# Kernel optimization log

Hardware: AMD Instinct MI355X
Metric: run time of the kernel (lower is better)

The kernel has to match this reference:

```python
import jax, jax.numpy as jnp
import numpy as np

N_EMBD = 1024
N_HEAD = 16
B, T = 2, 2048
LN_EPS = 1e-5


def _linear_params(key, d_in, d_out):
    k1, k2 = jax.random.split(key)
    bound = 1.0 / np.sqrt(d_in)
    W = jax.random.uniform(k1, (d_in, d_out), jnp.float32, -bound, bound)
    b = jax.random.uniform(k2, (d_out,), jnp.float32, -bound, bound)
    return W, b


def setup_inputs() -> dict:
    key = jax.random.key(0)
    ks = jax.random.split(key, 8)
    x = jax.random.normal(ks[0], (B, T, N_EMBD), jnp.float32)
    Wq, bq = _linear_params(ks[1], N_EMBD, N_EMBD)
    Wk, bk = _linear_params(ks[2], N_EMBD, N_EMBD)
    Wv, bv = _linear_params(ks[3], N_EMBD, N_EMBD)
    Wo, bo = _linear_params(ks[4], N_EMBD, N_EMBD)
    W1, b1 = _linear_params(ks[5], N_EMBD, 4 * N_EMBD)
    W2, b2 = _linear_params(ks[6], 4 * N_EMBD, N_EMBD)
    ln1_g = jnp.ones((N_EMBD,), jnp.float32)
    ln1_b = jnp.zeros((N_EMBD,), jnp.float32)
    ln2_g = jnp.ones((N_EMBD,), jnp.float32)
    ln2_b = jnp.zeros((N_EMBD,), jnp.float32)
    return dict(x=x, Wq=Wq, bq=bq, Wk=Wk, bk=bk, Wv=Wv, bv=bv, Wo=Wo, bo=bo,
                W1=W1, b1=b1, W2=W2, b2=b2,
                ln1_g=ln1_g, ln1_b=ln1_b, ln2_g=ln2_g, ln2_b=ln2_b)


def _layernorm(x, g, b):
    mu = jnp.mean(x, axis=-1, keepdims=True)
    var = jnp.mean(jnp.square(x - mu), axis=-1, keepdims=True)
    return (x - mu) * jax.lax.rsqrt(var + LN_EPS) * g + b


def _attention(x, Wq, bq, Wk, bk, Wv, bv, Wo, bo):
    Bsz, Tlen, C = x.shape
    hd = C // N_HEAD
    q = (x @ Wq + bq).reshape(Bsz, Tlen, N_HEAD, hd)
    k = (x @ Wk + bk).reshape(Bsz, Tlen, N_HEAD, hd)
    v = (x @ Wv + bv).reshape(Bsz, Tlen, N_HEAD, hd)
    scale = 1.0 / np.sqrt(hd)
    # NOTE: the original module's mask buffer is all ones -> masked_fill is a
    # no-op, so attention is FULL (non-causal) despite the class name.
    att = jnp.einsum('bqhd,bkhd->bhqk', q, k) * scale
    att = jax.nn.softmax(att, axis=-1)
    y = jnp.einsum('bhqk,bkhd->bqhd', att, v).reshape(Bsz, Tlen, C)
    return y @ Wo + bo


def reference(x, Wq, bq, Wk, bk, Wv, bv, Wo, bo, W1, b1, W2, b2,
              ln1_g, ln1_b, ln2_g, ln2_b):
    x = x + _attention(_layernorm(x, ln1_g, ln1_b), Wq, bq, Wk, bk, Wv, bv, Wo, bo)
    h = _layernorm(x, ln2_g, ln2_b)
    h = jax.nn.gelu(h @ W1 + b1, approximate=False) @ W2 + b2
    return x + h
```

## Files before the change

kernel.cpp:

```cpp
#include <hip/hip_runtime.h>
#include <hip/hip_bf16.h>
#include <math.h>


typedef __bf16 bf16x8 __attribute__((ext_vector_type(8)));
typedef float f32x4 __attribute__((ext_vector_type(4)));

__device__ __forceinline__ unsigned short f2bf(float f) {
  union { float f; unsigned int u; } v; v.f = f;
  unsigned int u = v.u;
  unsigned int r = (u + 0x7fffu + ((u >> 16) & 1u)) >> 16;
  return (unsigned short)r;
}

__device__ __forceinline__ unsigned int fbits(float f) {
  union { float f; unsigned int u; } v; v.f = f;
  return v.u;
}

__device__ __forceinline__ bf16x8 ld_bf16x8(const unsigned short* p) {
  union { uint4 u; bf16x8 v; } x;
  x.u = *(const uint4*)p;
  return x.v;
}

__device__ __forceinline__ float fast_exp2(float x) {
#if __has_builtin(__builtin_amdgcn_exp2f)
  return __builtin_amdgcn_exp2f(x);
#else
  return exp2f(x);
#endif
}

__device__ __forceinline__ void async_copy16(const void* g, void* l) {
  __builtin_amdgcn_global_load_lds(
      (const __attribute__((address_space(1))) void*)g,
      (__attribute__((address_space(3))) void*)l, 16, 0, 0);
}

__global__ __launch_bounds__(256) void transpose_cast_kernel(
    const float* __restrict__ W, unsigned short* __restrict__ Wt, int N, int K) {
  __shared__ unsigned short tile[32][33];
  const int n0 = blockIdx.x * 32, k0 = blockIdx.y * 32;
  const int t = threadIdx.x;
  const int r = t >> 3, cq = (t & 7) * 4;
  float4 v = *(const float4*)&W[(size_t)(k0 + r) * N + n0 + cq];
  tile[cq + 0][r] = f2bf(v.x);
  tile[cq + 1][r] = f2bf(v.y);
  tile[cq + 2][r] = f2bf(v.z);
  tile[cq + 3][r] = f2bf(v.w);
  __syncthreads();
  ushort4 o;
  o.x = tile[r][cq + 0];
  o.y = tile[r][cq + 1];
  o.z = tile[r][cq + 2];
  o.w = tile[r][cq + 3];
  *(ushort4*)&Wt[(size_t)(n0 + r) * K + k0 + cq] = o;
}

__global__ __launch_bounds__(256) void ln_kernel(
    const float* __restrict__ x, const float* __restrict__ g,
    const float* __restrict__ b, unsigned short* __restrict__ out) {
  const int row = blockIdx.x, t = threadIdx.x;
  const float4 v = ((const float4*)(x + (size_t)row * 1024))[t];
  float s = v.x + v.y + v.z + v.w;
  float s2 = v.x * v.x + v.y * v.y + v.z * v.z + v.w * v.w;
  for (int o = 32; o > 0; o >>= 1) {
    s += __shfl_xor(s, o, 64);
    s2 += __shfl_xor(s2, o, 64);
  }
  __shared__ float red[8];
  const int w = t >> 6;
  if ((t & 63) == 0) { red[w] = s; red[4 + w] = s2; }
  __syncthreads();
  s = red[0] + red[1] + red[2] + red[3];
  s2 = red[4] + red[5] + red[6] + red[7];
  const float mu = s * (1.f / 1024.f);
  const float var = s2 * (1.f / 1024.f) - mu * mu;
  const float rs = rsqrtf(var + 1e-5f);
  const float4 gg = ((const float4*)g)[t];
  const float4 bb = ((const float4*)b)[t];
  ushort4 o4;
  o4.x = f2bf((v.x - mu) * rs * gg.x + bb.x);
  o4.y = f2bf((v.y - mu) * rs * gg.y + bb.y);
  o4.z = f2bf((v.z - mu) * rs * gg.z + bb.z);
  o4.w = f2bf((v.w - mu) * rs * gg.w + bb.w);
  ((ushort4*)(out + (size_t)row * 1024))[t] = o4;
}

enum { MODE_QKV = 0, MODE_RES = 1, MODE_GELU = 2 };

#define QSCALE 0.18033688011112043f

template <int BM, int BN, int MODE>
__global__ __launch_bounds__(256) void gemm_kernel(
    const unsigned short* __restrict__ A, const unsigned short* __restrict__ Bt,
    const float* __restrict__ bias0, const float* __restrict__ bias1,
    const float* __restrict__ bias2, const float* __restrict__ residual,
    void* __restrict__ out0, void* __restrict__ out1, void* __restrict__ out2,
    int M, int N, int K) {
  constexpr int MI = BM / 32;
  constexpr int NI = BN / 32;
  __shared__ __align__(16) unsigned short As[3][2][BM * 32];
  __shared__ __align__(16) unsigned short Bs[3][2][BN * 32];
  const int t = threadIdx.x;

  const int MT = M / BM;
  const int MTX = MT >> 3;
  const int bid = blockIdx.x;
  const int xcd = bid & 7, local = bid >> 3;
  const int mt = xcd * MTX + (local % MTX);
  const int nt_ = local / MTX;
  const int m0 = mt * BM, n0 = nt_ * BN;

  const int l = t & 63, w = t >> 6;
  const int wm = (w >> 1) * (BM / 2), wn = (w & 1) * (BN / 2);
  const int lr = l & 15, lq = l >> 4;

  f32x4 acc[MI][NI];
#pragma unroll
  for (int i = 0; i < MI; i++)
#pragma unroll
    for (int j = 0; j < NI; j++) {
      f32x4 z = {0.f, 0.f, 0.f, 0.f};
      acc[i][j] = z;
    }

  auto issue = [&](int k0, int p) {
#pragma unroll
    for (int h = 0; h < 2; h++)
#pragma unroll
      for (int s = 0; s < BM / 64; s++) {
        const int c = t + s * 256;
        const int row = c >> 2, k8 = (c & 3) * 8;
        async_copy16(&A[(size_t)(m0 + row) * K + k0 + h * 32 + k8],
                     &As[p][h][c * 8]);
      }
#pragma unroll
    for (int h = 0; h < 2; h++)
#pragma unroll
      for (int s = 0; s < BN / 64; s++) {
        const int c = t + s * 256;
        const int row = c >> 2, k8 = (c & 3) * 8;
        async_copy16(&Bt[(size_t)(n0 + row) * K + k0 + h * 32 + k8],
                     &Bs[p][h][c * 8]);
      }
  };

  issue(0, 0);
  issue(64, 1);
  int p = 0;
  for (int k0 = 0; k0 < K; k0 += 64) {
    if (k0 + 64 < K)
      asm volatile("s_waitcnt vmcnt(6)\n\ts_barrier" ::: "memory");
    else
      asm volatile("s_waitcnt vmcnt(0)\n\ts_barrier" ::: "memory");
    if (k0 + 128 < K) {
      const int pn = p >= 1 ? p - 1 : 2;
      issue(k0 + 128, pn);
    }
#pragma unroll
    for (int kk = 0; kk < 2; kk++) {
      bf16x8 af[MI], bf[NI];
#pragma unroll
      for (int mi = 0; mi < MI; mi++)
        af[mi] = ld_bf16x8(&As[p][kk][(wm + mi * 16 + lr) * 32 + lq * 8]);
#pragma unroll
      for (int ni = 0; ni < NI; ni++)
        bf[ni] = ld_bf16x8(&Bs[p][kk][(wn + ni * 16 + lr) * 32 + lq * 8]);
#pragma unroll
      for (int mi = 0; mi < MI; mi++)
#pragma unroll
        for (int ni = 0; ni < NI; ni++)
          acc[mi][ni] = __builtin_amdgcn_mfma_f32_16x16x32_bf16(
              af[mi], bf[ni], acc[mi][ni], 0, 0, 0);
    }
    p = p < 2 ? p + 1 : 0;
  }

#pragma unroll
  for (int mi = 0; mi < MI; mi++) {
#pragma unroll
    for (int ni = 0; ni < NI; ni++) {
#pragma unroll
      for (int i = 0; i < 4; i++) {
        const int gm = m0 + wm + mi * 16 + lq * 4 + i;
        const int gn = n0 + wn + ni * 16 + lr;
        const float v = acc[mi][ni][i];
        if (MODE == MODE_QKV) {
          const int sel = gn >> 10, cn = gn & 1023;
          const int hh = cn >> 6, d = cn & 63;
          const int bb2 = gm >> 11, tok = gm & 2047;
          const size_t bh = (size_t)bb2 * 16 + hh;
          float u = v + (sel == 0 ? bias0 : (sel == 1 ? bias1 : bias2))[cn];
          if (sel == 0) {
            u *= QSCALE;
            const int qt = tok >> 7, r7 = tok & 127;
            const int ww = r7 >> 5, ss = (r7 >> 4) & 1, qlr = r7 & 15;
            const int kk = d >> 5, lq2 = (d >> 3) & 3, e = d & 7;
            const size_t idx =
                (((((bh * 16 + qt) * 4 + ww) * 2 + ss) * 2 + kk) << 9) +
                (lq2 * 16 + qlr) * 8 + e;
            ((unsigned short*)out0)[idx] = f2bf(u);
          } else if (sel == 1) {
            const int ktile = tok >> 6, r6 = tok & 63;
            const int nt2 = r6 >> 4, klr = r6 & 15;
            const int kk = d >> 5, lq2 = (d >> 3) & 3, e = d & 7;
            const size_t idx =
                ((((bh * 32 + ktile) * 4 + nt2) * 2 + kk) << 9) +
                (lq2 * 16 + klr) * 8 + e;
            ((unsigned short*)out1)[idx] = f2bf(u);
          } else {
            const int ktile = tok >> 6, r6 = tok & 63;
            const int kb = r6 >> 5, lq2 = (r6 >> 3) & 3, e = r6 & 7;
            const int nt2 = d >> 4, vlr = d & 15;
            const size_t idx =
                ((((bh * 32 + ktile) * 2 + kb) * 4 + nt2) << 9) +
                (lq2 * 16 + vlr) * 8 + e;
            ((unsigned short*)out2)[idx] = f2bf(u);
          }
        } else if (MODE == MODE_RES) {
          ((float*)out0)[(size_t)gm * N + gn] =
              v + bias0[gn] + residual[(size_t)gm * N + gn];
        } else {
          const float u = v + bias0[gn];
          const float ge = 0.5f * u * (1.f + erff(u * 0.70710678118654752f));
          ((unsigned short*)out0)[(size_t)gm * N + gn] = f2bf(ge);
        }
      }
    }
  }
}

__global__ __launch_bounds__(256) void attn_kernel(
    const unsigned short* __restrict__ Qp, const unsigned short* __restrict__ Kp,
    const unsigned short* __restrict__ Vp, unsigned short* __restrict__ O) {
  __shared__ __align__(16) unsigned short Ps[128 * 72];
  const int id = blockIdx.x;
  const int xcd = id & 7, loc = id >> 3;
  const int bh = xcd * 4 + (loc >> 4);
  const int qt = loc & 15;
  const int t = threadIdx.x, l = t & 63, w = t >> 6;
  const int lr = l & 15, lq = l >> 4;
  const int l8 = l * 8;
  const size_t rowBase = (size_t)(bh >> 4) * 2048;
  const int col0 = (bh & 15) * 64;

  const unsigned short* Qb_ = Qp + ((((size_t)bh * 16 + qt) * 4 + w) << 11);
  bf16x8 qf[2][2];
#pragma unroll
  for (int s = 0; s < 2; s++)
#pragma unroll
    for (int kk = 0; kk < 2; kk++)
      qf[s][kk] = ld_bf16x8(&Qb_[((s * 2 + kk) << 9) + l8]);

  const unsigned short* Kb_ = Kp + ((size_t)bh << 17);
  const unsigned short* Vb_ = Vp + ((size_t)bh << 17);

  bf16x8 kf[2][4];
#pragma unroll
  for (int nt = 0; nt < 4; nt++)
#pragma unroll
    for (int kk = 0; kk < 2; kk++)
      kf[kk][nt] = ld_bf16x8(&Kb_[((nt * 2 + kk) << 9) + l8]);

  f32x4 oacc[2][4];
#pragma unroll
  for (int s = 0; s < 2; s++)
#pragma unroll
    for (int nt = 0; nt < 4; nt++) {
      f32x4 z = {0.f, 0.f, 0.f, 0.f};
      oacc[s][nt] = z;
    }
  float lp[2] = {0.f, 0.f};

  for (int kt = 0; kt < 32; kt++) {
    const unsigned short* vtile = Vb_ + ((size_t)kt << 12);
    bf16x8 vf[2][4];
#pragma unroll
    for (int kb = 0; kb < 2; kb++)
#pragma unroll
      for (int nt = 0; nt < 4; nt++)
        vf[kb][nt] = ld_bf16x8(&vtile[((kb * 4 + nt) << 9) + l8]);

    f32x4 st[2][4];
#pragma unroll
    for (int s = 0; s < 2; s++)
#pragma unroll
      for (int nt = 0; nt < 4; nt++) {
        f32x4 z = {0.f, 0.f, 0.f, 0.f};
        st[s][nt] = z;
      }
#pragma unroll
    for (int nt = 0; nt < 4; nt++) {
      __builtin_amdgcn_s_setprio(1);
      st[0][nt] = __builtin_amdgcn_mfma_f32_16x16x32_bf16(kf[0][nt], qf[0][0], st[0][nt], 0, 0, 0);
      st[1][nt] = __builtin_amdgcn_mfma_f32_16x16x32_bf16(kf[0][nt], qf[1][0], st[1][nt], 0, 0, 0);
      st[0][nt] = __builtin_amdgcn_mfma_f32_16x16x32_bf16(kf[1][nt], qf[0][1], st[0][nt], 0, 0, 0);
      st[1][nt] = __builtin_amdgcn_mfma_f32_16x16x32_bf16(kf[1][nt], qf[1][1], st[1][nt], 0, 0, 0);
      __builtin_amdgcn_s_setprio(0);
    }

    const unsigned short* ktile_p = Kb_ + ((size_t)((kt + 1) & 31) << 12);
#pragma unroll
    for (int nt = 0; nt < 4; nt++)
#pragma unroll
      for (int kk = 0; kk < 2; kk++)
        kf[kk][nt] = ld_bf16x8(&ktile_p[((nt * 2 + kk) << 9) + l8]);

#pragma unroll
    for (int s = 0; s < 2; s++) {
      float rsum = 0.f;
#pragma unroll
      for (int nt = 0; nt < 4; nt++)
#pragma unroll
        for (int i = 0; i < 4; i++) {
          const float pv = fast_exp2(st[s][nt][i]);
          st[s][nt][i] = pv;
          rsum += pv;
        }
      lp[s] += rsum;
    }

#pragma unroll
    for (int s = 0; s < 2; s++)
#pragma unroll
      for (int nt = 0; nt < 4; nt++) {
        uint2 pk;
        pk.x = __builtin_amdgcn_perm(fbits(st[s][nt][1]), fbits(st[s][nt][0]), 0x07060302u);
        pk.y = __builtin_amdgcn_perm(fbits(st[s][nt][3]), fbits(st[s][nt][2]), 0x07060302u);
        *(uint2*)&Ps[(w * 32 + s * 16 + lr) * 72 + nt * 16 + lq * 4] = pk;
      }

#pragma unroll
    for (int kb = 0; kb < 2; kb++) {
      bf16x8 pf0 = ld_bf16x8(&Ps[(w * 32 + lr) * 72 + kb * 32 + lq * 8]);
      bf16x8 pf1 = ld_bf16x8(&Ps[(w * 32 + 16 + lr) * 72 + kb * 32 + lq * 8]);
      __builtin_amdgcn_s_setprio(1);
#pragma unroll
      for (int nt = 0; nt < 4; nt++) {
        oacc[0][nt] = __builtin_amdgcn_mfma_f32_16x16x32_bf16(pf0, vf[kb][nt], oacc[0][nt], 0, 0, 0);
        oacc[1][nt] = __builtin_amdgcn_mfma_f32_16x16x32_bf16(pf1, vf[kb][nt], oacc[1][nt], 0, 0, 0);
      }
      __builtin_amdgcn_s_setprio(0);
    }
  }

#pragma unroll
  for (int s = 0; s < 2; s++) {
    float li = lp[s];
    li += __shfl_xor(li, 16, 64);
    li += __shfl_xor(li, 32, 64);
    const float inv = 1.f / li;
#pragma unroll
    for (int nt = 0; nt < 4; nt++)
#pragma unroll
      for (int i = 0; i < 4; i++) {
        const size_t orow = rowBase + qt * 128 + w * 32 + s * 16 + lq * 4 + i;
        const int ocol = col0 + nt * 16 + lr;
        O[orow * 1024 + ocol] = f2bf(oacc[s][nt][i] * inv);
      }
  }
}

extern "C" void kernel_launch(void* const* d_in, const int* in_sizes, int n_in,
                              void* d_out, int out_size, void* d_ws, size_t ws_size,
                              hipStream_t stream) {
  const float* x    = (const float*)d_in[0];
  const float* Wq   = (const float*)d_in[1];
  const float* bq   = (const float*)d_in[2];
  const float* Wk   = (const float*)d_in[3];
  const float* bk   = (const float*)d_in[4];
  const float* Wv   = (const float*)d_in[5];
  const float* bv   = (const float*)d_in[6];
  const float* Wo   = (const float*)d_in[7];
  const float* bo   = (const float*)d_in[8];
  const float* W1   = (const float*)d_in[9];
  const float* b1   = (const float*)d_in[10];
  const float* W2   = (const float*)d_in[11];
  const float* b2   = (const float*)d_in[12];
  const float* ln1g = (const float*)d_in[13];
  const float* ln1b = (const float*)d_in[14];
  const float* ln2g = (const float*)d_in[15];
  const float* ln2b = (const float*)d_in[16];

  char* ws = (char*)d_ws;
  const size_t MB = 1024ull * 1024ull;
  unsigned short* WqT = (unsigned short*)(ws + 0 * MB);
  unsigned short* WkT = (unsigned short*)(ws + 2 * MB);
  unsigned short* WvT = (unsigned short*)(ws + 4 * MB);
  unsigned short* WoT = (unsigned short*)(ws + 6 * MB);
  unsigned short* W1T = (unsigned short*)(ws + 8 * MB);
  unsigned short* W2T = (unsigned short*)(ws + 16 * MB);
  unsigned short* xn  = (unsigned short*)(ws + 24 * MB);
  unsigned short* Qp  = (unsigned short*)(ws + 32 * MB);
  unsigned short* Kp  = (unsigned short*)(ws + 40 * MB);
  unsigned short* Vp  = (unsigned short*)(ws + 48 * MB);
  unsigned short* Ob  = (unsigned short*)(ws + 56 * MB);
  float*          x1  = (float*)(ws + 64 * MB);
  unsigned short* h2  = (unsigned short*)(ws + 80 * MB);
  unsigned short* Hb  = (unsigned short*)(ws + 24 * MB);

  const dim3 blk(256);

  transpose_cast_kernel<<<dim3(32, 32), blk, 0, stream>>>(Wq, WqT, 1024, 1024);
  transpose_cast_kernel<<<dim3(32, 32), blk, 0, stream>>>(Wk, WkT, 1024, 1024);
  transpose_cast_kernel<<<dim3(32, 32), blk, 0, stream>>>(Wv, WvT, 1024, 1024);
  transpose_cast_kernel<<<dim3(32, 32), blk, 0, stream>>>(Wo, WoT, 1024, 1024);
  transpose_cast_kernel<<<dim3(128, 32), blk, 0, stream>>>(W1, W1T, 4096, 1024);
  transpose_cast_kernel<<<dim3(32, 128), blk, 0, stream>>>(W2, W2T, 1024, 4096);

  ln_kernel<<<4096, blk, 0, stream>>>(x, ln1g, ln1b, xn);

  gemm_kernel<128, 64, MODE_QKV><<<dim3(32 * 48), blk, 0, stream>>>(
      xn, WqT, bq, bk, bv, nullptr, Qp, Kp, Vp, 4096, 3072, 1024);

  attn_kernel<<<dim3(512), blk, 0, stream>>>(Qp, Kp, Vp, Ob);

  gemm_kernel<128, 64, MODE_RES><<<dim3(32 * 16), blk, 0, stream>>>(
      Ob, WoT, bo, nullptr, nullptr, x, x1, nullptr, nullptr, 4096, 1024, 1024);

  ln_kernel<<<4096, blk, 0, stream>>>(x1, ln2g, ln2b, h2);

  gemm_kernel<128, 64, MODE_GELU><<<dim3(32 * 64), blk, 0, stream>>>(
      h2, W1T, b1, nullptr, nullptr, nullptr, Hb, nullptr, nullptr, 4096, 4096, 1024);

  gemm_kernel<128, 64, MODE_RES><<<dim3(32 * 16), blk, 0, stream>>>(
      Hb, W2T, b2, nullptr, nullptr, x1, (float*)d_out, nullptr, nullptr, 4096, 1024, 4096);
}
```

Before: 392.0 us.

## Use fragment-major LDS layout and 128x128 double-buffered tiles for QKV and FC1 GEMMs

Reorganizes the shared-memory tile layout so each 16-row MFMA fragment is stored contiguously, letting each lane read its operand with a linear lane*8 offset instead of a strided row address. Adds a buffer-count template parameter with a simpler double-buffered pipeline that uses __syncthreads. Switches the QKV and FC1 GEMMs to 128x128 tiles with two buffers, which raises per-block data reuse but halves the grid size and uses more registers per thread. The residual GEMMs keep 128x64 tiles with three buffers.

```diff
diff --git a/kernel.cpp b/kernel.cpp
--- a/kernel.cpp
+++ b/kernel.cpp
@@ -92,7 +92,7 @@
 
 #define QSCALE 0.18033688011112043f
 
-template <int BM, int BN, int MODE>
+template <int BM, int BN, int NBUF, int MODE>
 __global__ __launch_bounds__(256) void gemm_kernel(
     const unsigned short* __restrict__ A, const unsigned short* __restrict__ Bt,
     const float* __restrict__ bias0, const float* __restrict__ bias1,
@@ -101,8 +101,10 @@
     int M, int N, int K) {
   constexpr int MI = BM / 32;
   constexpr int NI = BN / 32;
-  __shared__ __align__(16) unsigned short As[3][2][BM * 32];
-  __shared__ __align__(16) unsigned short Bs[3][2][BN * 32];
+  constexpr int AG = BM / 16;
+  constexpr int BG = BN / 16;
+  __shared__ __align__(16) unsigned short As[NBUF][BM * 64];
+  __shared__ __align__(16) unsigned short Bs[NBUF][BN * 64];
   const int t = threadIdx.x;
 
   const int MT = M / BM;
@@ -128,46 +130,57 @@
 
   auto issue = [&](int k0, int p) {
 #pragma unroll
-    for (int h = 0; h < 2; h++)
-#pragma unroll
-      for (int s = 0; s < BM / 64; s++) {
-        const int c = t + s * 256;
-        const int row = c >> 2, k8 = (c & 3) * 8;
-        async_copy16(&A[(size_t)(m0 + row) * K + k0 + h * 32 + k8],
-                     &As[p][h][c * 8]);
-      }
-#pragma unroll
-    for (int h = 0; h < 2; h++)
-#pragma unroll
-      for (int s = 0; s < BN / 64; s++) {
-        const int c = t + s * 256;
-        const int row = c >> 2, k8 = (c & 3) * 8;
-        async_copy16(&Bt[(size_t)(n0 + row) * K + k0 + h * 32 + k8],
-                     &Bs[p][h][c * 8]);
-      }
+    for (int s = 0; s < BM / 32; s++) {
+      const int c = t + s * 256;
+      const int cl = c & 63;
+      const int g = (c >> 6) % AG;
+      const int kk = (c >> 6) / AG;
+      const int row = g * 16 + (cl & 15);
+      const int col = kk * 32 + (cl >> 4) * 8;
+      async_copy16(&A[(size_t)(m0 + row) * K + k0 + col], &As[p][c * 8]);
+    }
+#pragma unroll
+    for (int s = 0; s < BN / 32; s++) {
+      const int c = t + s * 256;
+      const int cl = c & 63;
+      const int g = (c >> 6) % BG;
+      const int kk = (c >> 6) / BG;
+      const int row = g * 16 + (cl & 15);
+      const int col = kk * 32 + (cl >> 4) * 8;
+      async_copy16(&Bt[(size_t)(n0 + row) * K + k0 + col], &Bs[p][c * 8]);
+    }
   };
 
-  issue(0, 0);
-  issue(64, 1);
   int p = 0;
+  if constexpr (NBUF == 3) {
+    issue(0, 0);
+    issue(64, 1);
+  } else {
+    issue(0, 0);
+  }
+
   for (int k0 = 0; k0 < K; k0 += 64) {
-    if (k0 + 64 < K)
-      asm volatile("s_waitcnt vmcnt(6)\n\ts_barrier" ::: "memory");
-    else
-      asm volatile("s_waitcnt vmcnt(0)\n\ts_barrier" ::: "memory");
-    if (k0 + 128 < K) {
-      const int pn = p >= 1 ? p - 1 : 2;
-      issue(k0 + 128, pn);
+    if constexpr (NBUF == 3) {
+      if (k0 + 64 < K)
+        asm volatile("s_waitcnt vmcnt(6)\n\ts_barrier" ::: "memory");
+      else
+        asm volatile("s_waitcnt vmcnt(0)\n\ts_barrier" ::: "memory");
+      if (k0 + 128 < K) issue(k0 + 128, p >= 1 ? p - 1 : 2);
+    } else {
+      __syncthreads();
+      if (k0 + 64 < K) issue(k0 + 64, p ^ 1);
     }
 #pragma unroll
     for (int kk = 0; kk < 2; kk++) {
       bf16x8 af[MI], bf[NI];
 #pragma unroll
       for (int mi = 0; mi < MI; mi++)
-        af[mi] = ld_bf16x8(&As[p][kk][(wm + mi * 16 + lr) * 32 + lq * 8]);
+        af[mi] = ld_bf16x8(
+            &As[p][((kk * AG + (w >> 1) * MI + mi) << 9) + l * 8]);
 #pragma unroll
       for (int ni = 0; ni < NI; ni++)
-        bf[ni] = ld_bf16x8(&Bs[p][kk][(wn + ni * 16 + lr) * 32 + lq * 8]);
+        bf[ni] = ld_bf16x8(
+            &Bs[p][((kk * BG + (w & 1) * NI + ni) << 9) + l * 8]);
 #pragma unroll
       for (int mi = 0; mi < MI; mi++)
 #pragma unroll
@@ -175,7 +188,10 @@
           acc[mi][ni] = __builtin_amdgcn_mfma_f32_16x16x32_bf16(
               af[mi], bf[ni], acc[mi][ni], 0, 0, 0);
     }
-    p = p < 2 ? p + 1 : 0;
+    if constexpr (NBUF == 3)
+      p = p < 2 ? p + 1 : 0;
+    else
+      p ^= 1;
   }
 
 #pragma unroll
@@ -412,19 +428,19 @@
 
   ln_kernel<<<4096, blk, 0, stream>>>(x, ln1g, ln1b, xn);
 
-  gemm_kernel<128, 64, MODE_QKV><<<dim3(32 * 48), blk, 0, stream>>>(
+  gemm_kernel<128, 128, 2, MODE_QKV><<<dim3(32 * 24), blk, 0, stream>>>(
       xn, WqT, bq, bk, bv, nullptr, Qp, Kp, Vp, 4096, 3072, 1024);
 
   attn_kernel<<<dim3(512), blk, 0, stream>>>(Qp, Kp, Vp, Ob);
 
-  gemm_kernel<128, 64, MODE_RES><<<dim3(32 * 16), blk, 0, stream>>>(
+  gemm_kernel<128, 64, 3, MODE_RES><<<dim3(32 * 16), blk, 0, stream>>>(
       Ob, WoT, bo, nullptr, nullptr, x, x1, nullptr, nullptr, 4096, 1024, 1024);
 
   ln_kernel<<<4096, blk, 0, stream>>>(x1, ln2g, ln2b, h2);
 
-  gemm_kernel<128, 64, MODE_GELU><<<dim3(32 * 64), blk, 0, stream>>>(
+  gemm_kernel<128, 128, 2, MODE_GELU><<<dim3(32 * 32), blk, 0, stream>>>(
       h2, W1T, b1, nullptr, nullptr, nullptr, Hb, nullptr, nullptr, 4096, 4096, 1024);
 
-  gemm_kernel<128, 64, MODE_RES><<<dim3(32 * 16), blk, 0, stream>>>(
+  gemm_kernel<128, 64, 3, MODE_RES><<<dim3(32 * 16), blk, 0, stream>>>(
       Hb, W2T, b2, nullptr, nullptr, x1, (float*)d_out, nullptr, nullptr, 4096, 1024, 4096);
 }
```

Measured after the change: 452.0 us. +15.3%, slower.
